# Optimization experiments

Hardware: AMD Instinct MI355X
Metric: run time of the kernel (lower is better)

The kernel has to match this reference:

```python
import jax, jax.numpy as jnp
import numpy as np

DILATIONS = [[1, 2], [4, 8]]
H = 512      # state_hsize
D_IN = 128   # input_size + exogenous_size
OUT = 48     # output_size
T, B = 256, 128


def _lstm(x, W_ih, W_hh, b_ih, b_hh):
    # x: (T2, B2, D). Standard torch nn.LSTM math, gate order i, f, g, o.
    h0 = jnp.zeros((x.shape[1], W_hh.shape[1]), x.dtype)
    b = b_ih + b_hh

    def step(carry, xt):
        h, c = carry
        g = xt @ W_ih.T + h @ W_hh.T + b
        i, f, gg, o = jnp.split(g, 4, axis=-1)
        c = jax.nn.sigmoid(f) * c + jax.nn.sigmoid(i) * jnp.tanh(gg)
        h = jax.nn.sigmoid(o) * jnp.tanh(c)
        return (h, c), h

    _, ys = jax.lax.scan(step, (h0, h0), x)
    return ys


def _drnn_layer(x, rate, W_ih, W_hh, b_ih, b_hh):
    # Dilated RNN layer: interleave time into the batch dim by `rate`,
    # run a plain LSTM, then de-interleave (zalando DRNN scheme).
    T0, B0, D0 = x.shape
    pad = (-T0) % rate
    if pad:
        x = jnp.concatenate([x, jnp.zeros((pad, B0, D0), x.dtype)], 0)
    Tp = T0 + pad
    dil = x.reshape(Tp // rate, rate * B0, D0)   # dil[t, j*B0+b] = x[t*rate+j, b]
    out = _lstm(dil, W_ih, W_hh, b_ih, b_hh)     # (Tp//rate, rate*B0, H)
    out = out.reshape(Tp // rate, rate, B0, -1).reshape(Tp, B0, -1)
    return out[:T0]


def _forward(input_data, Wih, Whh, bih, bhh, mlp_w, mlp_b, adapter_w, adapter_b):
    x = input_data
    k = 0
    for stack_idx, dils in enumerate(DILATIONS):
        residual = x
        h = x
        for d in dils:
            h = _drnn_layer(h, d, Wih[k], Whh[k], bih[k], bhh[k])
            k += 1
        x = h + residual if stack_idx > 0 else h
    x = jnp.tanh(x @ mlp_w.T + mlp_b)
    return x @ adapter_w.T + adapter_b


def setup_inputs() -> dict:
    key = jax.random.key(0)
    ks = jax.random.split(key, 32)

    def gn(k, shape, s=0.05):
        return (jax.random.normal(k, shape) * s).astype(jnp.float32)

    inp = {"input_data": jax.random.normal(ks[0], (T, B, D_IN), jnp.float32)}
    cell_in = [D_IN, H, H, H]  # input dim of each of the 4 LSTM cells
    for i, d in enumerate(cell_in):
        inp[f"W_ih_{i}"] = gn(ks[1 + 4 * i], (4 * H, d))
        inp[f"W_hh_{i}"] = gn(ks[2 + 4 * i], (4 * H, H))
        inp[f"b_ih_{i}"] = gn(ks[3 + 4 * i], (4 * H,))
        inp[f"b_hh_{i}"] = gn(ks[4 + 4 * i], (4 * H,))
    inp["mlp_w"] = gn(ks[20], (H, H))
    inp["mlp_b"] = gn(ks[21], (H,))
    inp["adapter_w"] = gn(ks[22], (OUT, H))
    inp["adapter_b"] = gn(ks[23], (OUT,))
    return inp


def reference(input_data, W_ih_0, W_hh_0, b_ih_0, b_hh_0,
              W_ih_1, W_hh_1, b_ih_1, b_hh_1,
              W_ih_2, W_hh_2, b_ih_2, b_hh_2,
              W_ih_3, W_hh_3, b_ih_3, b_hh_3,
              mlp_w, mlp_b, adapter_w, adapter_b):
    Wih = [W_ih_0, W_ih_1, W_ih_2, W_ih_3]
    Whh = [W_hh_0, W_hh_1, W_hh_2, W_hh_3]
    bih = [b_ih_0, b_ih_1, b_ih_2, b_ih_3]
    bhh = [b_hh_0, b_hh_1, b_hh_2, b_hh_3]
    return _forward(input_data, Wih, Whh, bih, bhh, mlp_w, mlp_b, adapter_w, adapter_b)
```

## Files before the change

### kernel.cpp

```cpp
#include <hip/hip_runtime.h>

#define TPB 512
#define SPIN_BOUND (1u << 20)

typedef _Float16 h8 __attribute__((ext_vector_type(8)));
typedef float f4 __attribute__((ext_vector_type(4)));
typedef unsigned long long u64;

__device__ __forceinline__ float sigf(float x) { return 1.f / (1.f + __expf(-x)); }
__device__ __forceinline__ float tanhfast(float x) { return 2.f / (1.f + __expf(-2.f * x)) - 1.f; }

#define MF(acc, a, b) acc = __builtin_amdgcn_mfma_f32_16x16x32_f16(a, b, acc, 0, 0, 0)

__device__ __forceinline__ void vm0() { asm volatile("s_waitcnt vmcnt(0)" ::: "memory"); }
__device__ __forceinline__ void l1inv() { asm volatile("buffer_inv sc0" ::: "memory"); }
__device__ __forceinline__ void lgkm0() { asm volatile("s_waitcnt lgkmcnt(0)" ::: "memory"); }



__global__ void prep_conv(const float* __restrict__ in, const float* __restrict__ mlpw,
                          const float* __restrict__ adpw,
                          _Float16* __restrict__ seqX, _Float16* __restrict__ mlpW16,
                          _Float16* __restrict__ adpW16)
{
    const int NIN = 256 * 128 * 128;
    const int NM = 512 * 512;
    const int NA = 48 * 512;
    int i = blockIdx.x * blockDim.x + threadIdx.x;
    const int stride = gridDim.x * blockDim.x;
    for (; i < NIN + NM + NA; i += stride) {
        if (i < NIN) seqX[i] = (_Float16)in[i];
        else if (i < NIN + NM) mlpW16[i - NIN] = (_Float16)mlpw[i - NIN];
        else adpW16[i - NIN - NM] = (_Float16)adpw[i - NIN - NM];
    }
}

__global__ void prep_bias(const float* __restrict__ a0, const float* __restrict__ b0,
                          const float* __restrict__ a1, const float* __restrict__ b1,
                          const float* __restrict__ a2, const float* __restrict__ b2,
                          const float* __restrict__ a3, const float* __restrict__ b3,
                          float* __restrict__ biasSum)
{
    int i = blockIdx.x * blockDim.x + threadIdx.x;
    if (i >= 8192) return;
    const int c = i >> 11, j = i & 2047;
    const float* A = (c == 0) ? a0 : (c == 1) ? a1 : (c == 2) ? a2 : a3;
    const float* B = (c == 0) ? b0 : (c == 1) ? b1 : (c == 2) ? b2 : b3;
    biasSum[i] = A[j] + B[j];
}

__global__ void prep_w(const float* __restrict__ wih0, const float* __restrict__ whh0,
                       const float* __restrict__ wih1, const float* __restrict__ whh1,
                       const float* __restrict__ wih2, const float* __restrict__ whh2,
                       const float* __restrict__ wih3, const float* __restrict__ whh3,
                       _Float16* __restrict__ Wprep)
{
    const size_t N0 = (size_t)2048 * 640;
    const size_t N1 = (size_t)2048 * 1024;
    const size_t total = N0 + 3 * N1;
    size_t i = (size_t)blockIdx.x * blockDim.x + threadIdx.x;
    const size_t stride = (size_t)gridDim.x * blockDim.x;
    for (; i < total; i += stride) {
        int cell; size_t off;
        if (i < N0) { cell = 0; off = i; }
        else { cell = 1 + (int)((i - N0) / N1); off = (i - N0) % N1; }
        const int K = cell ? 1024 : 640;
        const int Din = cell ? 512 : 128;
        const int k = (int)(off % K);
        const int rowIdx = (int)(off / K);
        const int p = rowIdx >> 6;
        const int row64 = rowIdx & 63;
        const int q = row64 >> 4;
        const int gRow = q * 512 + p * 16 + (row64 & 15);
        const float* wih = (cell == 0) ? wih0 : (cell == 1) ? wih1 : (cell == 2) ? wih2 : wih3;
        const float* whh = (cell == 0) ? whh0 : (cell == 1) ? whh1 : (cell == 2) ? whh2 : whh3;
        const float v = (k < Din) ? wih[(size_t)gRow * Din + k]
                                  : whh[(size_t)gRow * 512 + (k - Din)];
        Wprep[i] = (_Float16)v;
    }
}


#define SCR_OFF   131072
#define SCRT_OFF  147456
#define MISC_OFF  151552

template<int CELL, int KH, bool XH>
__device__ __forceinline__ void run_cell(
    const _Float16* __restrict__ src, _Float16* __restrict__ dstX,
    const _Float16* __restrict__ wbase, const float* __restrict__ biasSum,
    unsigned* __restrict__ cellFlags, char* smem,
    const int rg, const int p, const int tid, const int lane, const int wave)
{
    constexpr int Din = (CELL == 0) ? 128 : 512;
    constexpr int K = Din + 512;
    constexpr int Bd = 128 << CELL;
    constexpr int PBd = Bd / 2;
    constexpr int Td = 256 >> CELL;
    constexpr int r = Bd >> 3;
    constexpr int nMt = r >> 4;
    constexpr int ldsRow = K * 2;
    constexpr int NKX = Din >> 5;
    constexpr int NXW = NKX / KH;
    constexpr int NHW = 16 / KH;
    constexpr int B1 = (NHW > 8) ? 8 : NHW;
    constexpr int B2 = NHW - B1;
    constexpr int NCOMP = nMt * KH;

    const int colsel = lane & 15;
    const int kq = lane >> 4;
    const int rowBase = rg * r;

    {
        const _Float16* wsl = wbase + (size_t)p * 64 * K;
        constexpr int kcN = K >> 3;
        for (int i = tid; i < 64 * kcN; i += TPB) {
            const int row = i / kcN;
            const int kc = i - row * kcN;
            h8 v = *(const h8*)(wsl + (size_t)row * K + (kc << 3));
            *(h8*)(smem + row * ldsRow + ((kc << 4) ^ ((row & 7) << 4))) = v;
        }
    }
    __syncthreads();

    const int mt = wave / KH;
    const int kh = wave % KH;
    const bool busy = (wave < NCOMP);

    const int xlo = kh * NXW;
    const int hlo = kh * NHW;

    const float bq0 = biasSum[CELL * 2048 + 0 * 512 + p * 16 + colsel];
    const float bq1 = biasSum[CELL * 2048 + 1 * 512 + p * 16 + colsel];
    const float bq2 = biasSum[CELL * 2048 + 2 * 512 + p * 16 + colsel];
    const float bq3 = biasSum[CELL * 2048 + 3 * 512 + p * 16 + colsel];

    const int arow = rowBase + mt * 16 + colsel;

    unsigned* line = cellFlags + (rg * 8 + mt) * 256;
    unsigned* myFlag = line + p * 8;
    float* scr = (float*)(smem + SCR_OFF);
    char* scrT = smem + SCRT_OFF + mt * 512;

    float cr[4] = {0.f, 0.f, 0.f, 0.f};
    bool dead = false;
    h8 xr[(NXW > 0) ? NXW : 1];

    const size_t hOff = (size_t)arow * 16 + (size_t)(kq & 1) * 8 + (size_t)(kq >> 1) * (Bd * 16);
    const int tOff = (arow >= PBd) ? 1 : 0;
    const size_t xBase = (size_t)(arow - tOff * PBd) * 16
                       + (size_t)(kq & 1) * 8 + (size_t)(kq >> 1) * (PBd * 16);

    auto ldB = [&](int kbyte, int rrow) -> h8 {
        return *(const h8*)(smem + rrow * ldsRow + (kbyte ^ ((rrow & 7) << 4)));
    };

    auto wait_line = [&](unsigned tgt) {
        if (dead) return;
        const volatile unsigned* fp = (const volatile unsigned*)(line + (lane & 31) * 8);
        unsigned n = 0;
        for (;;) {
            if (__all((int)(*fp >= tgt))) return;
            l1inv();
            __builtin_amdgcn_s_sleep(1);
            if (++n > SPIN_BOUND) { dead = true; return; }
        }
    };
    auto wait_own = [&](unsigned tgt) {
        if (dead) return;
        const volatile unsigned* f0 = (const volatile unsigned*)myFlag;
        if (*f0 >= tgt) return;
        unsigned n = 0;
        for (;;) {
            l1inv();
            if (*f0 >= tgt) return;
            __builtin_amdgcn_s_sleep(1);
            if (++n > SPIN_BOUND) { dead = true; return; }
        }
    };

    auto x_issue = [&](int t) {
        if constexpr (XH) {
            const char* xp = (const char*)src
                + ((size_t)(2 * t + tOff) * (32 * PBd * 16) + xBase) * 2;
            #pragma unroll
            for (int i = 0; i < NXW; ++i)
                xr[i] = *(const h8*)(xp + (size_t)(xlo + i) * (PBd * 64));
        } else {
            const _Float16* ap = src + (size_t)t * Bd * Din + (size_t)arow * Din + (kq << 3);
            #pragma unroll
            for (int i = 0; i < NXW; ++i)
                xr[i] = *(const h8*)(ap + ((xlo + i) << 5));
        }
    };
    auto x_compute = [&](f4 (&C)[4]) {
        #pragma unroll
        for (int g = 0; g < 4; ++g) C[g] = (f4){0.f, 0.f, 0.f, 0.f};
        #pragma unroll
        for (int i = 0; i < NXW; ++i) {
            const int kbyte = (((xlo + i) << 5) + (kq << 3)) << 1;
            h8 bf0 = ldB(kbyte, colsel);
            h8 bf1 = ldB(kbyte, 16 + colsel);
            h8 bf2 = ldB(kbyte, 32 + colsel);
            h8 bf3 = ldB(kbyte, 48 + colsel);
            MF(C[0], xr[i], bf0); MF(C[1], xr[i], bf1);
            MF(C[2], xr[i], bf2); MF(C[3], xr[i], bf3);
        }
    };
    auto h_mfma = [&](h8 a, int ks, f4 (&C)[4]) {
        const int kbyte = (Din + (ks << 5) + (kq << 3)) << 1;
        h8 bf0 = ldB(kbyte, colsel);
        h8 bf1 = ldB(kbyte, 16 + colsel);
        h8 bf2 = ldB(kbyte, 32 + colsel);
        h8 bf3 = ldB(kbyte, 48 + colsel);
        MF(C[0], a, bf0); MF(C[1], a, bf1); MF(C[2], a, bf2); MF(C[3], a, bf3);
    };
    auto writeScr = [&](f4 (&C)[4]) {
        const int slot = (mt * (KH - 1) + (kh - 1)) * 4;
        #pragma unroll
        for (int g = 0; g < 4; ++g)
            *(f4*)(scr + (size_t)((slot + g) * 64 + lane) * 4) = C[g];
    };
    auto finish = [&](int t, f4 (&C)[4]) {
        if constexpr (KH > 1) {
            #pragma unroll
            for (int s = 0; s < KH - 1; ++s)
                #pragma unroll
                for (int g = 0; g < 4; ++g)
                    C[g] += *(const f4*)(scr + (size_t)(((mt * (KH - 1) + s) * 4 + g) * 64 + lane) * 4);
        }
        _Float16 hf[4];
        #pragma unroll
        for (int j = 0; j < 4; ++j) {
            const float gi = C[0][j] + bq0;
            const float gf = C[1][j] + bq1;
            const float gg = C[2][j] + bq2;
            const float go = C[3][j] + bq3;
            const float cc = sigf(gf) * cr[j] + sigf(gi) * tanhfast(gg);
            cr[j] = cc;
            hf[j] = (_Float16)(sigf(go) * tanhfast(cc));
        }
        #pragma unroll
        for (int j = 0; j < 4; ++j)
            *(_Float16*)(scrT + (kq * 4 + j) * 32 + colsel * 2) = hf[j];
        lgkm0();
        const u64 v = *(const u64*)(scrT + (lane >> 2) * 32 + (lane & 3) * 8);
        const size_t Ebase = ((size_t)t * 32 + p) * (size_t)(Bd * 16)
                           + (size_t)(rowBase + mt * 16) * 16;
        *(u64*)((char*)dstX + Ebase * 2 + (size_t)lane * 8) = v;
        vm0();
        if (lane == 0) *(volatile unsigned*)myFlag = (unsigned)(t + 1);
    };

    f4 acc[4];
    h8 hrA[B1];
    h8 hrB[(B2 > 0) ? B2 : 1];
    if (busy) x_issue(0);

    for (int t = 0; t < Td; ++t) {
        const char* hXp = (const char*)dstX + ((size_t)(t - 1) * (32 * Bd * 16) + hOff) * 2;
        if (busy && t > 0) {
            if constexpr (KH > 1) { if (kh != 0) wait_own((unsigned)t); }
            wait_line((unsigned)t);
            #pragma unroll
            for (int i = 0; i < B1; ++i)
                hrA[i] = *(const h8*)(hXp + (size_t)(hlo + i) * (Bd * 64));
        }
        if (busy) {
            x_compute(acc);
            if (t > 0) {
                if constexpr (B2 > 0) {
                    #pragma unroll
                    for (int i = 0; i < B2; ++i)
                        hrB[i] = *(const h8*)(hXp + (size_t)(hlo + B1 + i) * (Bd * 64));
                }
                #pragma unroll
                for (int i = 0; i < B1; ++i) h_mfma(hrA[i], hlo + i, acc);
                if constexpr (B2 > 0) {
                    #pragma unroll
                    for (int i = 0; i < B2; ++i) h_mfma(hrB[i], hlo + B1 + i, acc);
                }
            }
        }
        if constexpr (KH > 1) {
            if (busy && kh != 0) writeScr(acc);
            __syncthreads();
        }
        if (busy && kh == 0) finish(t, acc);
        if (busy && t + 1 < Td) x_issue(t + 1);
    }
    vm0();
}


__global__ __launch_bounds__(TPB) void drnn_persist(
    const _Float16* __restrict__ seqX,
    _Float16* __restrict__ seq0X,
    _Float16* __restrict__ seq1X,
    _Float16* __restrict__ seq2X,
    _Float16* __restrict__ seq3X,
    const _Float16* __restrict__ Wprep,
    const float* __restrict__ biasSum,
    unsigned* __restrict__ syncc)
{
    extern __shared__ char smem[];
    const int tid = threadIdx.x;
    const int lane = tid & 63;
    const int wave = tid >> 6;

    unsigned* s_misc = (unsigned*)(smem + MISC_OFF);

    if (tid == 0) {
        unsigned xcc;
        asm volatile("s_getreg_b32 %0, hwreg(HW_REG_XCC_ID)" : "=s"(xcc));
        xcc &= 7u;
        unsigned slot = __hip_atomic_fetch_add(syncc + 512u + 64u * xcc, 1u,
                                               __ATOMIC_RELAXED, __HIP_MEMORY_SCOPE_AGENT);
        s_misc[0] = (xcc << 5) | (slot & 31u);
    }
    __syncthreads();
    const unsigned rgp = s_misc[0];
    __syncthreads();
    const int rg = rgp >> 5;
    const int p = rgp & 31;

    unsigned* cellCnt = syncc;
    unsigned* flags = syncc + 4096;

    auto cell_barrier = [&](int cellIdx, unsigned TdPrev, int nMtPrev, unsigned* flagsPrev) {
        __syncthreads();
        if (p == 0 && tid < 32 * nMtPrev) {
            const volatile unsigned* fp =
                (const volatile unsigned*)(flagsPrev + (rg * 8 + (tid >> 5)) * 256 + (tid & 31) * 8);
            unsigned n = 0;
            for (;;) {
                l1inv();
                if (*fp >= TdPrev) break;
                __builtin_amdgcn_s_sleep(1);
                if (++n > SPIN_BOUND) break;
            }
        }
        __syncthreads();
        if (tid == 0) {
            if (p == 0)
                __hip_atomic_fetch_add(cellCnt, 1u, __ATOMIC_RELEASE, __HIP_MEMORY_SCOPE_AGENT);
            unsigned n = 0;
            while (__hip_atomic_load(cellCnt, __ATOMIC_RELAXED, __HIP_MEMORY_SCOPE_AGENT)
                   < (unsigned)(8 * cellIdx)) {
                __builtin_amdgcn_s_sleep(1);
                if (++n > SPIN_BOUND) break;
            }
            (void)__hip_atomic_load(cellCnt, __ATOMIC_ACQUIRE, __HIP_MEMORY_SCOPE_AGENT);
        }
        __syncthreads();
        l1inv();
    };

    run_cell<0, 2, false>(seqX,  seq0X, Wprep,                        biasSum, flags + 0 * 16384, smem, rg, p, tid, lane, wave);
    cell_barrier(1, 256u, 1, flags + 0 * 16384);
    run_cell<1, 2, true >(seq0X, seq1X, Wprep + (size_t)2048 * 640,   biasSum, flags + 1 * 16384, smem, rg, p, tid, lane, wave);
    cell_barrier(2, 128u, 2, flags + 1 * 16384);
    run_cell<2, 2, true >(seq1X, seq2X, Wprep + (size_t)2048 * 1664,  biasSum, flags + 2 * 16384, smem, rg, p, tid, lane, wave);
    cell_barrier(3, 64u, 4, flags + 2 * 16384);
    run_cell<3, 1, true >(seq2X, seq3X, Wprep + (size_t)2048 * 2688,  biasSum, flags + 3 * 16384, smem, rg, p, tid, lane, wave);
}


__global__ __launch_bounds__(256) void head_kernel(
    const _Float16* __restrict__ seq1X,
    const _Float16* __restrict__ seq3X,
    const _Float16* __restrict__ mlpW16,
    const float* __restrict__ mlp_b,
    const _Float16* __restrict__ adpW16,
    const float* __restrict__ adp_b,
    float* __restrict__ out)
{
    extern __shared__ char smem[];
    const int tid = threadIdx.x;
    const int lane = tid & 63, wave = tid >> 6;
    const int colsel = lane & 15, kq = lane >> 4;
    const size_t row0 = (size_t)blockIdx.x * 64 + wave * 16;

    h8 aR[16];
    {
        const size_t R = row0 + colsel;
        const size_t off1 = ((R >> 8) * 32 + (size_t)(kq >> 1)) * 4096
                          + (R & 255) * 16 + (size_t)(kq & 1) * 8;
        const size_t off3 = ((R >> 10) * 32 + (size_t)(kq >> 1)) * 16384
                          + (R & 1023) * 16 + (size_t)(kq & 1) * 8;
        #pragma unroll
        for (int ks = 0; ks < 16; ++ks) {
            h8 a1 = *(const h8*)(seq1X + off1 + (size_t)ks * 8192);
            h8 a3 = *(const h8*)(seq3X + off3 + (size_t)ks * 32768);
            aR[ks] = a1 + a3;
        }
    }
    for (int nt = 0; nt < 32; ++nt) {
        f4 acc = {0.f, 0.f, 0.f, 0.f};
        const int brow = nt * 16 + colsel;
        #pragma unroll
        for (int ks = 0; ks < 16; ++ks) {
            const int kb = ks * 32 + kq * 8;
            h8 b = *(const h8*)(mlpW16 + (size_t)brow * 512 + kb);
            acc = __builtin_amdgcn_mfma_f32_16x16x32_f16(aR[ks], b, acc, 0, 0, 0);
        }
        const int n = nt * 16 + colsel;
        const float bn = mlp_b[n];
        const int lrow0 = wave * 16 + kq * 4;
        #pragma unroll
        for (int j = 0; j < 4; ++j) {
            const float y = tanhfast(acc[j] + bn);
            const int row = lrow0 + j;
            *(_Float16*)(smem + row * 1024 + ((n * 2) ^ ((row & 7) << 4))) = (_Float16)y;
        }
    }
    __syncthreads();
    f4 acc0 = {0.f,0.f,0.f,0.f}, acc1 = {0.f,0.f,0.f,0.f}, acc2 = {0.f,0.f,0.f,0.f};
    const int arow = wave * 16 + colsel;
    #pragma unroll
    for (int ks = 0; ks < 16; ++ks) {
        const int kb = ks * 32 + kq * 8;
        h8 a = *(const h8*)(smem + arow * 1024 + ((kb * 2) ^ ((arow & 7) << 4)));
        h8 b0 = *(const h8*)(adpW16 + (size_t)(colsel) * 512 + kb);
        h8 b1 = *(const h8*)(adpW16 + (size_t)(16 + colsel) * 512 + kb);
        h8 b2 = *(const h8*)(adpW16 + (size_t)(32 + colsel) * 512 + kb);
        acc0 = __builtin_amdgcn_mfma_f32_16x16x32_f16(a, b0, acc0, 0, 0, 0);
        acc1 = __builtin_amdgcn_mfma_f32_16x16x32_f16(a, b1, acc1, 0, 0, 0);
        acc2 = __builtin_amdgcn_mfma_f32_16x16x32_f16(a, b2, acc2, 0, 0, 0);
    }
    const size_t orow0 = row0 + kq * 4;
    #pragma unroll
    for (int j = 0; j < 4; ++j) {
        out[(orow0 + j) * 48 + colsel]      = acc0[j] + adp_b[colsel];
        out[(orow0 + j) * 48 + 16 + colsel] = acc1[j] + adp_b[16 + colsel];
        out[(orow0 + j) * 48 + 32 + colsel] = acc2[j] + adp_b[32 + colsel];
    }
}


extern "C" void kernel_launch(void* const* d_in, const int* in_sizes, int n_in,
                              void* d_out, int out_size, void* d_ws, size_t ws_size,
                              hipStream_t stream)
{
    (void)in_sizes; (void)n_in; (void)out_size; (void)ws_size;
    const float* input = (const float*)d_in[0];
    const float* Wih[4]; const float* Whh[4]; const float* Bih[4]; const float* Bhh[4];
    for (int i = 0; i < 4; ++i) {
        Wih[i] = (const float*)d_in[1 + 4 * i];
        Whh[i] = (const float*)d_in[2 + 4 * i];
        Bih[i] = (const float*)d_in[3 + 4 * i];
        Bhh[i] = (const float*)d_in[4 + 4 * i];
    }
    const float* mlpw = (const float*)d_in[17];
    const float* mlpb = (const float*)d_in[18];
    const float* adpw = (const float*)d_in[19];
    const float* adpb = (const float*)d_in[20];
    float* out = (float*)d_out;

    char* ws = (char*)d_ws;
    size_t off = 0;
    auto alloc = [&](size_t bytes) -> char* {
        char* ptr = ws + off;
        off += (bytes + 255) & ~(size_t)255;
        return ptr;
    };
    const size_t SEQB = (size_t)32768 * 512 * 2;
    const size_t SYNC_BYTES = (size_t)(4096 + 4 * 16384) * 4;
    unsigned* syncc   = (unsigned*)alloc(SYNC_BYTES);
    _Float16* seqX    = (_Float16*)alloc((size_t)32768 * 128 * 2);
    _Float16* seq0X   = (_Float16*)alloc(SEQB);
    _Float16* seq1X   = (_Float16*)alloc(SEQB);
    _Float16* seq2X   = (_Float16*)alloc(SEQB);
    _Float16* seq3X   = (_Float16*)alloc(SEQB);
    _Float16* Wprep   = (_Float16*)alloc((size_t)2048 * 3712 * 2);
    float*    biasSum = (float*)alloc(8192 * 4);
    _Float16* mlpW16  = (_Float16*)alloc((size_t)262144 * 2);
    _Float16* adpW16  = (_Float16*)alloc((size_t)24576 * 2);

    hipMemsetAsync(syncc, 0, SYNC_BYTES, stream);
    prep_conv<<<2048, 256, 0, stream>>>(input, mlpw, adpw, seqX, mlpW16, adpW16);
    prep_bias<<<32, 256, 0, stream>>>(Bih[0], Bhh[0], Bih[1], Bhh[1],
                                      Bih[2], Bhh[2], Bih[3], Bhh[3], biasSum);
    prep_w<<<4096, 256, 0, stream>>>(Wih[0], Whh[0], Wih[1], Whh[1],
                                     Wih[2], Whh[2], Wih[3], Whh[3], Wprep);

    const int ldsBytes = MISC_OFF + 128;
    hipFuncSetAttribute((const void*)drnn_persist,
                        hipFuncAttributeMaxDynamicSharedMemorySize, ldsBytes);
    hipFuncSetAttribute((const void*)head_kernel,
                        hipFuncAttributeMaxDynamicSharedMemorySize, 65536);

    drnn_persist<<<256, TPB, ldsBytes, stream>>>(seqX, seq0X, seq1X, seq2X, seq3X,
                                                 Wprep, biasSum, syncc);
    head_kernel<<<512, 256, 65536, stream>>>(seq1X, seq3X, mlpW16, mlpb, adpW16, adpb, out);
}
```

Baseline: 2.002 ms.

## Wait per h-chunk flag and pipeline loads with MFMAs in staggered order

Replaces the single wait on all 32 producer flags of a line with per-chunk waits, so each k-chunk of the previous hidden state is consumed as soon as its two producers have published. Each block starts at a different chunk offset based on its column slice, spreading contention, and keeps a two-deep load/MFMA pipeline. This aims to overlap the recurrent dependency wait with compute instead of stalling until the slowest producer finishes. It adds more flag polls and cache invalidations per step, and it relies on the flag-to-chunk mapping being exact for correctness.

```diff
diff --git a/kernel.cpp b/kernel.cpp
--- a/kernel.cpp
+++ b/kernel.cpp
@@ -103,8 +103,6 @@
     constexpr int NKX = Din >> 5;
     constexpr int NXW = NKX / KH;
     constexpr int NHW = 16 / KH;
-    constexpr int B1 = (NHW > 8) ? 8 : NHW;
-    constexpr int B2 = NHW - B1;
     constexpr int NCOMP = nMt * KH;
 
     const int colsel = lane & 15;
@@ -129,6 +127,7 @@
 
     const int xlo = kh * NXW;
     const int hlo = kh * NHW;
+    const int start = (p >> 1) % NHW;
 
     const float bq0 = biasSum[CELL * 2048 + 0 * 512 + p * 16 + colsel];
     const float bq1 = biasSum[CELL * 2048 + 1 * 512 + p * 16 + colsel];
@@ -150,18 +149,21 @@
     const int tOff = (arow >= PBd) ? 1 : 0;
     const size_t xBase = (size_t)(arow - tOff * PBd) * 16
                        + (size_t)(kq & 1) * 8 + (size_t)(kq >> 1) * (PBd * 16);
+    const int fpar = (kq >> 1);
 
     auto ldB = [&](int kbyte, int rrow) -> h8 {
         return *(const h8*)(smem + rrow * ldsRow + (kbyte ^ ((rrow & 7) << 4)));
     };
 
-    auto wait_line = [&](unsigned tgt) {
+    auto wait_chunk = [&](int ks, unsigned tgt) {
         if (dead) return;
-        const volatile unsigned* fp = (const volatile unsigned*)(line + (lane & 31) * 8);
+        const volatile unsigned* fp =
+            (const volatile unsigned*)(line + (2 * ks + fpar) * 8);
+        if (__all((int)(*fp >= tgt))) return;
         unsigned n = 0;
         for (;;) {
+            l1inv();
             if (__all((int)(*fp >= tgt))) return;
-            l1inv();
             __builtin_amdgcn_s_sleep(1);
             if (++n > SPIN_BOUND) { dead = true; return; }
         }
@@ -253,33 +255,37 @@
     };
 
     f4 acc[4];
-    h8 hrA[B1];
-    h8 hrB[(B2 > 0) ? B2 : 1];
+    h8 hr[NHW];
+    int ksv[NHW];
     if (busy) x_issue(0);
 
     for (int t = 0; t < Td; ++t) {
         const char* hXp = (const char*)dstX + ((size_t)(t - 1) * (32 * Bd * 16) + hOff) * 2;
         if (busy && t > 0) {
             if constexpr (KH > 1) { if (kh != 0) wait_own((unsigned)t); }
-            wait_line((unsigned)t);
             #pragma unroll
-            for (int i = 0; i < B1; ++i)
-                hrA[i] = *(const h8*)(hXp + (size_t)(hlo + i) * (Bd * 64));
+            for (int i = 0; i < 2; ++i) {
+                int s = start + i; if (s >= NHW) s -= NHW;
+                const int ks = hlo + s;
+                ksv[i] = ks;
+                wait_chunk(ks, (unsigned)t);
+                hr[i] = *(const h8*)(hXp + (size_t)ks * (Bd * 64));
+            }
         }
         if (busy) {
             x_compute(acc);
             if (t > 0) {
-                if constexpr (B2 > 0) {
-                    #pragma unroll
-                    for (int i = 0; i < B2; ++i)
-                        hrB[i] = *(const h8*)(hXp + (size_t)(hlo + B1 + i) * (Bd * 64));
+                #pragma unroll
+                for (int i = 2; i < NHW; ++i) {
+                    int s = start + i; if (s >= NHW) s -= NHW;
+                    const int ks = hlo + s;
+                    ksv[i] = ks;
+                    wait_chunk(ks, (unsigned)t);
+                    hr[i] = *(const h8*)(hXp + (size_t)ks * (Bd * 64));
+                    h_mfma(hr[i - 2], ksv[i - 2], acc);
                 }
-                #pragma unroll
-                for (int i = 0; i < B1; ++i) h_mfma(hrA[i], hlo + i, acc);
-                if constexpr (B2 > 0) {
-                    #pragma unroll
-                    for (int i = 0; i < B2; ++i) h_mfma(hrB[i], hlo + B1 + i, acc);
-                }
+                h_mfma(hr[NHW - 2], ksv[NHW - 2], acc);
+                h_mfma(hr[NHW - 1], ksv[NHW - 1], acc);
             }
         }
         if constexpr (KH > 1) {
```

Measured after the change: 2.438 ms. +21.8%, slower.
